# Kernel optimization log

Hardware: AMD Instinct MI355X
Metric: run time of the kernel (lower is better)

The kernel has to match this reference:

```python
import jax, jax.numpy as jnp
from jax import lax
import numpy as np

EPS = 1e-5
SCALE, K_UP = 2, 5  # CARAFE defaults


def conv(x, w, pad=0):
    return lax.conv_general_dilated(x, w, (1, 1), [(pad, pad), (pad, pad)],
                                    dimension_numbers=('NCHW', 'OIHW', 'NCHW'))


def bn(x, g, b, m, v):
    # eval-mode BatchNorm2d
    inv = g * lax.rsqrt(v + EPS)
    return x * inv[None, :, None, None] + (b - m * inv)[None, :, None, None]


def carafe(X, comp_w, comp_g, comp_bt, comp_m, comp_v, enc_w, enc_g, enc_bt, enc_m, enc_v):
    b, c, h, w = X.shape
    k2 = K_UP * K_UP
    W = jax.nn.relu(bn(conv(X, comp_w), comp_g, comp_bt, comp_m, comp_v))  # (b, c_mid, h, w)
    W = bn(conv(W, enc_w, pad=1), enc_g, enc_bt, enc_m, enc_v)             # (b, k2*SCALE^2, h, w)
    # PixelShuffle(SCALE): (b, k2*r^2, h, w) -> (b, k2, h*r, w*r)
    W = W.reshape(b, k2, SCALE, SCALE, h, w).transpose(0, 1, 4, 2, 5, 3)
    W = W.reshape(b, k2, h * SCALE, w * SCALE)
    W = jax.nn.softmax(W, axis=1)
    # nearest upsample by SCALE
    Xu = jnp.repeat(jnp.repeat(X, SCALE, axis=2), SCALE, axis=3)
    pad = (K_UP // 2) * SCALE
    Xp = jnp.pad(Xu, ((0, 0), (0, 0), (pad, pad), (pad, pad)))
    h_, w_ = h * SCALE, w * SCALE
    # Unfold(kernel=K_UP, dilation=SCALE): channel-major then kernel index, matching torch
    patches = jnp.stack([Xp[:, :, i * SCALE:i * SCALE + h_, j * SCALE:j * SCALE + w_]
                         for i in range(K_UP) for j in range(K_UP)], axis=2)  # (b,c,k2,h_,w_)
    return jnp.einsum('bkhw,bckhw->bchw', W, patches)


def setup_inputs():
    key = jax.random.key(0)
    ks = iter(jax.random.split(key, 80))
    nk = lambda: next(ks)
    P = lambda shape, s=0.05: jax.random.normal(nk(), shape, jnp.float32) * s
    d = {}
    B, C_out = 4, 64
    cins = [128, 256, 512]
    hw = [(96, 160), (48, 80), (24, 40)]
    for i, (ci, (h, w)) in enumerate(zip(cins, hw)):
        d[f'x{i}'] = jax.random.normal(nk(), (B, ci, h, w), jnp.float32)
        d[f'lat{i}_w'] = P((C_out, ci, 1, 1))
        d[f'lat{i}_b'] = P((C_out,))
        d[f'fpn{i}_w'] = P((C_out, C_out, 3, 3))
        d[f'fpn{i}_b'] = P((C_out,))
    k2s2 = (SCALE * K_UP) ** 2
    for u in range(2):
        d[f'u{u}_comp_w'] = P((C_out, C_out, 1, 1))
        d[f'u{u}_enc_w'] = P((k2s2, C_out, 3, 3))
        for nm, c in [('comp', C_out), ('enc', k2s2)]:
            d[f'u{u}_{nm}_g'] = 1.0 + P((c,))
            d[f'u{u}_{nm}_bt'] = P((c,))
            d[f'u{u}_{nm}_m'] = P((c,))
            d[f'u{u}_{nm}_v'] = jax.random.uniform(nk(), (c,), jnp.float32, 0.5, 1.5)
    return d


def reference(x0, x1, x2,
              lat0_w, lat0_b, fpn0_w, fpn0_b,
              lat1_w, lat1_b, fpn1_w, fpn1_b,
              lat2_w, lat2_b, fpn2_w, fpn2_b,
              u0_comp_w, u0_enc_w, u0_comp_g, u0_comp_bt, u0_comp_m, u0_comp_v,
              u0_enc_g, u0_enc_bt, u0_enc_m, u0_enc_v,
              u1_comp_w, u1_enc_w, u1_comp_g, u1_comp_bt, u1_comp_m, u1_comp_v,
              u1_enc_g, u1_enc_bt, u1_enc_m, u1_enc_v):
    lat = [conv(x, w) + b[None, :, None, None] for x, w, b in
           [(x0, lat0_w, lat0_b), (x1, lat1_w, lat1_b), (x2, lat2_w, lat2_b)]]
    # top-down pathway with CARAFE upsampling
    lat[1] = lat[1] + carafe(lat[2], u1_comp_w, u1_comp_g, u1_comp_bt, u1_comp_m, u1_comp_v,
                             u1_enc_w, u1_enc_g, u1_enc_bt, u1_enc_m, u1_enc_v)
    lat[0] = lat[0] + carafe(lat[1], u0_comp_w, u0_comp_g, u0_comp_bt, u0_comp_m, u0_comp_v,
                             u0_enc_w, u0_enc_g, u0_enc_bt, u0_enc_m, u0_enc_v)
    outs = tuple(conv(l, w, pad=1) + b[None, :, None, None] for l, w, b in
                 [(lat[0], fpn0_w, fpn0_b), (lat[1], fpn1_w, fpn1_b), (lat[2], fpn2_w, fpn2_b)])
    return outs
```

## Files before the change

kernel.cpp:

```cpp
#include <hip/hip_runtime.h>

#define BN_EPS 1e-5f

typedef __attribute__((ext_vector_type(8))) short bf16x8;
typedef __attribute__((ext_vector_type(4))) float f32x4;

__device__ __forceinline__ unsigned short f2bf(float f) {
    unsigned u = __float_as_uint(f);
    return (unsigned short)((u + 0x7fffu + ((u >> 16) & 1u)) >> 16);
}
__device__ __forceinline__ unsigned packbf(float lo, float hi) {
    return ((unsigned)f2bf(hi) << 16) | (unsigned)f2bf(lo);
}

__global__ __launch_bounds__(256)
void prep_weights(const float* __restrict__ w0, const float* __restrict__ w1,
                  const float* __restrict__ w2, const float* __restrict__ w3,
                  const float* __restrict__ w4, unsigned short* __restrict__ dst,
                  const float* __restrict__ v0, const float* __restrict__ v1,
                  const float* __restrict__ v2, const float* __restrict__ v3,
                  const float* __restrict__ v4, unsigned short* __restrict__ dst1)
{
    int z = blockIdx.y;
    int i = blockIdx.x * 256 + threadIdx.x;
    if (z < 5) {
        const float* src; unsigned short* d; int C_out, COP;
        if (z < 3) {
            COP = 64; C_out = 64;
            src = (z == 0) ? w0 : (z == 1 ? w1 : w2);
            d = dst + z * 36864;
            if (i >= 36864) return;
        } else {
            COP = 112; C_out = 100;
            src = (z == 3) ? w3 : w4;
            d = dst + 110592 + (z - 3) * 64512;
            if (i >= 64512) return;
        }
        int tap = i / (COP * 64);
        int rem = i - tap * (COP * 64);
        int co = rem >> 6, ci = rem & 63;
        float v = (co < C_out) ? src[((size_t)co * 64 + ci) * 9 + tap] : 0.f;
        d[i] = f2bf(v);
    } else {
        int zz = z - 5;
        const float* s; int n; int off;
        if (zz == 0)      { s = v0; n = 8192;  off = 0; }
        else if (zz == 1) { s = v1; n = 16384; off = 8192; }
        else if (zz == 2) { s = v2; n = 32768; off = 24576; }
        else if (zz == 3) { s = v3; n = 4096;  off = 57344; }
        else              { s = v4; n = 4096;  off = 61440; }
        if (i >= n) return;
        dst1[off + i] = f2bf(s[i]);
    }
}

template<int COP, int CSPLIT, int MODE>
__device__ __forceinline__
void conv3x3_body(int rem, int TX, unsigned short* xs,
                  const unsigned* __restrict__ xp,
                  const unsigned short* __restrict__ wt,
                  const float* __restrict__ p0, const float* __restrict__ p1,
                  const float* __restrict__ p2, const float* __restrict__ p3,
                  float* __restrict__ out, int H, int W, int C_out)
{
    constexpr int NP = 324;
    constexpr int CT = COP / 16;
    static_assert(CT == CSPLIT, "CPB must be 1 (R1/R2 VGPR cliff)");

    int cs = rem % CSPLIT;
    int b  = (rem / CSPLIT) & 3;
    int t  = rem / (CSPLIT * 4);
    int x0 = (t % TX) * 16, y0 = (t / TX) * 16;

    int tid  = threadIdx.x;
    int lane = tid & 63, wid = tid >> 6;
    int lrow = lane >> 4, lcol = lane & 15;
    int HWp = H * W;

    int co0 = cs * 16;
    bool colok = (x0 + lcol) < W;

    f32x4 accA[2], accB[2];
#pragma unroll
    for (int rr = 0; rr < 2; ++rr) {
        accA[rr] = (f32x4){0.f, 0.f, 0.f, 0.f};
        accB[rr] = (f32x4){0.f, 0.f, 0.f, 0.f};
    }

    unsigned int* wsl = (unsigned int*)xs;

#pragma unroll 1
    for (int kb = 0; kb < 2; ++kb) {
        if (kb) __syncthreads();
        for (int p = tid; p < NP; p += 256) {
            int py = p / 18, px = p - py * 18;
            int gy = y0 + py - 1, gx = x0 + px - 1;
            bool ok = (gy >= 0) && (gy < H) && (gx >= 0) && (gx < W);
            const unsigned* gpp = xp + ((size_t)b * 32 + kb * 16) * HWp
                                     + (size_t)gy * W + gx;
#pragma unroll 8
            for (int cp = 0; cp < 16; ++cp) {
                unsigned pk = ok ? gpp[(size_t)cp * HWp] : 0u;
                wsl[((cp >> 2) * NP + p) * 4 + (cp & 3)] = pk;
            }
        }
        __syncthreads();

        bf16x8 a[9];
        const unsigned short* wl = wt + ((size_t)co0 + lcol) * 64 + kb * 32 + lrow * 8;
#pragma unroll
        for (int t9 = 0; t9 < 9; ++t9)
            a[t9] = *(const bf16x8*)(wl + (size_t)t9 * COP * 64);

#pragma unroll
        for (int rr = 0; rr < 2; ++rr) {
            int r0 = wid + rr * 8;
#pragma unroll
            for (int t9 = 0; t9 < 9; ++t9) {
                int dy = t9 / 3, dx = t9 - dy * 3;
                int g0 = lrow * NP + (r0 + dy) * 18 + lcol + dx;
                bf16x8 b0 = *(const bf16x8*)(xs + (size_t)g0 * 8);
                accA[rr] = __builtin_amdgcn_mfma_f32_16x16x32_bf16(a[t9], b0, accA[rr], 0, 0, 0);
                bf16x8 b1 = *(const bf16x8*)(xs + ((size_t)g0 + 4 * 18) * 8);
                accB[rr] = __builtin_amdgcn_mfma_f32_16x16x32_bf16(a[t9], b1, accB[rr], 0, 0, 0);
            }
        }
    }

    float sc[4], sh[4];
#pragma unroll
    for (int rg = 0; rg < 4; ++rg) {
        int co = co0 + lrow * 4 + rg;
        int cc = (co < C_out) ? co : 0;
        if (MODE == 0) { sc[rg] = 1.f; sh[rg] = p0[cc]; }
        else {
            float inv = p0[cc] * rsqrtf(p3[cc] + BN_EPS);
            sc[rg] = inv; sh[rg] = p1[cc] - p2[cc] * inv;
        }
    }
#pragma unroll
    for (int rr = 0; rr < 2; ++rr) {
        int r0 = wid + rr * 8;
        int yA = y0 + r0, yB = y0 + r0 + 4;
#pragma unroll
        for (int rg = 0; rg < 4; ++rg) {
            int co = co0 + lrow * 4 + rg;
            if (colok && co < C_out) {
                float* oc = out + (((size_t)b * C_out + co) * H) * W + x0 + lcol;
                if (yA < H) oc[(size_t)yA * W] = accA[rr][rg] * sc[rg] + sh[rg];
                if (yB < H) oc[(size_t)yB * W] = accB[rr][rg] * sc[rg] + sh[rg];
            }
        }
    }
}

__global__ __launch_bounds__(256, 6)
void enc_fpn(int encBlocks,
             const unsigned* __restrict__ cxp, const unsigned short* __restrict__ wt_e,
             const float* __restrict__ g, const float* __restrict__ bt,
             const float* __restrict__ m, const float* __restrict__ v,
             float* __restrict__ enc_out, int He, int We, int TXe,
             const unsigned* __restrict__ xp, const unsigned short* __restrict__ wt_f,
             const float* __restrict__ bias, float* __restrict__ fout,
             int Hf, int Wf, int TXf)
{
    __shared__ unsigned short xs[4 * 324 * 8];
    int f = blockIdx.x;
    if (f < encBlocks)
        conv3x3_body<112, 7, 1>(f, TXe, xs, cxp, wt_e,
                                g, bt, m, v, enc_out, He, We, 100);
    else
        conv3x3_body<64, 4, 0>(f - encBlocks, TXf, xs, xp, wt_f,
                               bias, nullptr, nullptr, nullptr, fout, Hf, Wf, 64);
}

__global__ __launch_bounds__(256, 6)
void fpn_multi(const unsigned* __restrict__ l0p, const unsigned short* __restrict__ wt0,
               const float* __restrict__ b0, float* __restrict__ o0)
{
    __shared__ unsigned short xs[4 * 324 * 8];
    conv3x3_body<64, 4, 0>(blockIdx.x, 10, xs, l0p, wt0,
                           b0, nullptr, nullptr, nullptr, o0, 96, 160, 64);
}

template<int C_IN, int KSPLIT, int NPX, int MODE, bool MIRROR>
__device__ __forceinline__
void conv1x1_body(int f, unsigned short* xs,
                  const float* __restrict__ x, const unsigned short* __restrict__ wb,
                  const float* __restrict__ p0, const float* __restrict__ p1,
                  const float* __restrict__ p2, const float* __restrict__ p3,
                  float* __restrict__ out, unsigned* __restrict__ outp, int HW)
{
    constexpr int NT = NPX / 16;
    constexpr int KLEN = C_IN / KSPLIT;
    constexpr int QUADS = NPX / 4;
    int nb = HW / NPX;
    int px0 = (f % nb) * NPX;
    int ks  = (f / nb) % KSPLIT;
    int b   = f / (nb * KSPLIT);

    int tid = threadIdx.x;
    int lane = tid & 63, wid = tid >> 6;
    int lrow = lane >> 4, lcol = lane & 15;
    const float* xb = x + (size_t)b * C_IN * HW + px0;

    f32x4 acc[NT];
#pragma unroll
    for (int nt = 0; nt < NT; ++nt) acc[nt] = (f32x4){0.f, 0.f, 0.f, 0.f};

    for (int cc = 0; cc < KLEN; cc += 32) {
        if (cc) __syncthreads();
        int cb = ks * KLEN + cc;
        for (int j = tid; j < 16 * QUADS; j += 256) {
            int q  = j & (QUADS - 1);
            int cp = j / QUADS;
            int px = q * 4;
            const float* s0 = xb + (size_t)(cb + 2 * cp) * HW + px;
            float4 v0 = *(const float4*)s0;
            float4 v1 = *(const float4*)(s0 + HW);
            unsigned* wv = (unsigned*)xs + ((size_t)(cp >> 2) * NPX + px) * 4 + (cp & 3);
            wv[0]  = packbf(v0.x, v1.x);
            wv[4]  = packbf(v0.y, v1.y);
            wv[8]  = packbf(v0.z, v1.z);
            wv[12] = packbf(v0.w, v1.w);
        }
        __syncthreads();

        bf16x8 a = *(const bf16x8*)(wb + (size_t)(wid * 16 + lcol) * C_IN + cb + lrow * 8);
#pragma unroll
        for (int nt = 0; nt < NT; ++nt) {
            bf16x8 bf = *(const bf16x8*)(xs + ((size_t)lrow * NPX + nt * 16 + lcol) * 8);
            acc[nt] = __builtin_amdgcn_mfma_f32_16x16x32_bf16(a, bf, acc[nt], 0, 0, 0);
        }
    }

    if (KSPLIT == 1) {
        if (MIRROR) {
#pragma unroll
            for (int rg = 0; rg < 4; rg += 2) {
                int co = wid * 16 + lrow * 4 + rg;
                float inv0 = p0[co] * rsqrtf(p3[co] + BN_EPS);
                float sh0  = p1[co] - p2[co] * inv0;
                float inv1 = p0[co + 1] * rsqrtf(p3[co + 1] + BN_EPS);
                float sh1  = p1[co + 1] - p2[co + 1] * inv1;
                unsigned* pp = outp + ((size_t)(b * 32 + (co >> 1))) * HW + px0;
#pragma unroll
                for (int nt = 0; nt < NT; ++nt) {
                    float r0 = fmaxf(acc[nt][rg] * inv0 + sh0, 0.f);
                    float r1 = fmaxf(acc[nt][rg + 1] * inv1 + sh1, 0.f);
                    pp[nt * 16 + lcol] = packbf(r0, r1);
                }
            }
        } else {
#pragma unroll
            for (int rg = 0; rg < 4; ++rg) {
                int co = wid * 16 + lrow * 4 + rg;
                float scale, shift;
                if (MODE == 0) { scale = 1.f; shift = p0[co]; }
                else {
                    float inv = p0[co] * rsqrtf(p3[co] + BN_EPS);
                    scale = inv; shift = p1[co] - p2[co] * inv;
                }
                float* op = out + ((size_t)(b * 64 + co)) * HW + px0;
#pragma unroll
                for (int nt = 0; nt < NT; ++nt) {
                    float r = acc[nt][rg] * scale + shift;
                    if (MODE == 1) r = fmaxf(r, 0.f);
                    op[nt * 16 + lcol] = r;
                }
            }
        }
    } else {
#pragma unroll
        for (int rg = 0; rg < 4; ++rg) {
            int co = wid * 16 + lrow * 4 + rg;
            float* op = out + (((size_t)(ks * 4 + b)) * 64 + co) * HW + px0;
#pragma unroll
            for (int nt = 0; nt < NT; ++nt)
                op[nt * 16 + lcol] = acc[nt][rg];
        }
    }
}

template<int C_IN, int KSPLIT, int NPX, int MODE, bool MIRROR>
__global__ __launch_bounds__(256, 4)
void conv1x1_mfma(const float* __restrict__ x, const unsigned short* __restrict__ wb,
                  const float* __restrict__ p0, const float* __restrict__ p1,
                  const float* __restrict__ p2, const float* __restrict__ p3,
                  float* __restrict__ out, unsigned* __restrict__ outp, int HW)
{
    __shared__ __align__(16) unsigned short xs[4 * NPX * 8];
    int nb = HW / NPX;
    int f = blockIdx.x + nb * (blockIdx.y + KSPLIT * blockIdx.z);
    conv1x1_body<C_IN, KSPLIT, NPX, MODE, MIRROR>(f, xs, x, wb, p0, p1, p2, p3, out, outp, HW);
}

__global__ __launch_bounds__(256, 4)
void lat_multi(const float* __restrict__ x0, const unsigned short* __restrict__ w0,
               const float* __restrict__ b0, float* __restrict__ lat0,
               const float* __restrict__ x1, const unsigned short* __restrict__ w1,
               float* __restrict__ part1,
               const float* __restrict__ x2, const unsigned short* __restrict__ w2,
               float* __restrict__ part2)
{
    __shared__ __align__(16) unsigned short xs[4 * 128 * 8];
    int f = blockIdx.x;
    if (f < 480)
        conv1x1_body<128, 1, 128, 0, false>(f, xs, x0, w0, b0, nullptr, nullptr, nullptr, lat0, nullptr, 15360);
    else if (f < 720)
        conv1x1_body<256, 2, 128, 0, false>(f - 480, xs, x1, w1, nullptr, nullptr, nullptr, nullptr, part1, nullptr, 3840);
    else
        conv1x1_body<512, 4, 64, 0, false>(f - 720, xs, x2, w2, nullptr, nullptr, nullptr, nullptr, part2, nullptr, 960);
}

template<int KSPLIT>
__device__ __forceinline__
void reduce_body(int f, const float* __restrict__ part, const float* __restrict__ bias,
                 float* __restrict__ out, int HW, int N4)
{
    int i = f * 256 + threadIdx.x;
    if (i >= N4) return;
    size_t base = (size_t)i * 4;
    int co = (int)((base / (size_t)HW) & 63);
    size_t stride = (size_t)HW << 8;
    float4 s = *(const float4*)(part + base);
#pragma unroll
    for (int ks = 1; ks < KSPLIT; ++ks) {
        float4 t = *(const float4*)(part + (size_t)ks * stride + base);
        s.x += t.x; s.y += t.y; s.z += t.z; s.w += t.w;
    }
    float bv = bias[co];
    s.x += bv; s.y += bv; s.z += bv; s.w += bv;
    *(float4*)(out + base) = s;
}

__device__ __forceinline__
void reduce_pack4(int f, const float* __restrict__ part, const float* __restrict__ bias,
                  float* __restrict__ out, unsigned* __restrict__ outp, int HW, int N)
{
    int i = f * 256 + threadIdx.x;
    if (i >= N) return;
    int q = HW >> 2;
    int pxq  = i % q;
    int rest = i / q;
    int cp = rest & 31, b = rest >> 5;
    size_t off = (size_t)pxq * 4;
    size_t c0 = ((size_t)(b * 64 + 2 * cp)) * HW + off;
    size_t stride = (size_t)HW << 8;
    float4 s0 = *(const float4*)(part + c0);
    float4 s1 = *(const float4*)(part + c0 + HW);
#pragma unroll
    for (int ks = 1; ks < 4; ++ks) {
        float4 t0 = *(const float4*)(part + (size_t)ks * stride + c0);
        float4 t1 = *(const float4*)(part + (size_t)ks * stride + c0 + HW);
        s0.x += t0.x; s0.y += t0.y; s0.z += t0.z; s0.w += t0.w;
        s1.x += t1.x; s1.y += t1.y; s1.z += t1.z; s1.w += t1.w;
    }
    float bv0 = bias[2 * cp], bv1 = bias[2 * cp + 1];
    s0.x += bv0; s0.y += bv0; s0.z += bv0; s0.w += bv0;
    s1.x += bv1; s1.y += bv1; s1.z += bv1; s1.w += bv1;
    *(float4*)(out + c0) = s0;
    *(float4*)(out + c0 + HW) = s1;
    uint4 pk;
    pk.x = packbf(s0.x, s1.x);
    pk.y = packbf(s0.y, s1.y);
    pk.z = packbf(s0.z, s1.z);
    pk.w = packbf(s0.w, s1.w);
    *(uint4*)(outp + ((size_t)(b * 32 + cp)) * HW + off) = pk;
}

__global__ __launch_bounds__(256)
void reduce_multi(const float* __restrict__ part1, const float* __restrict__ b1,
                  float* __restrict__ lat1,
                  const float* __restrict__ part2, const float* __restrict__ b2,
                  float* __restrict__ lat2, unsigned* __restrict__ lat2p)
{
    int f = blockIdx.x;
    if (f < 960) reduce_body<2>(f, part1, b1, lat1, 3840, 245760);
    else         reduce_pack4(f - 960, part2, b2, lat2, lat2p, 960, 30720);
}

template<int CGS, bool WF32>
__global__ __launch_bounds__(256, 4)
void carafe_kernel(const float* __restrict__ src, const float* __restrict__ logits,
                   float* __restrict__ dst, unsigned* __restrict__ dstp, int h, int w)
{
    constexpr int SW = 12, NPX = 144;
    constexpr int CH = 64 / CGS;
    constexpr int CS = CH + 4;
    __shared__ float ls[NPX * CS];

    int tid = threadIdx.x;
    int x0 = blockIdx.x * 16, y0 = blockIdx.y * 16;
    int b  = blockIdx.z / CGS;
    int cs = blockIdx.z % CGS;
    int H = 2 * h, W = 2 * w;
    int xs0 = (x0 >> 1) - 2, ys0 = (y0 >> 1) - 2;
    size_t hw = (size_t)h * w;
    const float* sb = src + ((size_t)(b * 64 + cs * CH)) * hw;

    for (int i = tid; i < NPX * CH; i += 256) {
        int c = i / NPX, p = i - c * NPX;
        int yy = p / SW, xx = p - yy * SW;
        int sy = ys0 + yy, sx = xs0 + xx;
        float v = 0.f;
        if (sy >= 0 && sy < h && sx >= 0 && sx < w)
            v = sb[(size_t)c * hw + (size_t)sy * w + sx];
        ls[p * CS + c] = v;
    }
    __syncthreads();

    int lx = tid & 15, ty = tid >> 4;
    int x = x0 + lx, y = y0 + ty;
    int xw = x >> 1, yh = y >> 1;
    int par = (y & 1) * 2 + (x & 1);

    const float* lp = logits + ((size_t)(b * 100 + par) * h + yh) * w + xw;
    float l[25];
    float mx = -1e30f;
#pragma unroll
    for (int k = 0; k < 25; ++k) {
        l[k] = lp[(size_t)(4 * k) * hw];
        mx = fmaxf(mx, l[k]);
    }
    float s = 0.f;
#pragma unroll
    for (int k = 0; k < 25; ++k) {
        l[k] = __expf(l[k] - mx);
        s += l[k];
    }
    float invs = 1.f / s;
#pragma unroll
    for (int k = 0; k < 25; ++k) l[k] *= invs;

    int pb = (yh - ys0 - 2) * SW + (xw - xs0 - 2);

#pragma unroll 1
    for (int cg = 0; cg < CH / 16; ++cg) {
        float acc[16];
#pragma unroll
        for (int c = 0; c < 16; ++c) acc[c] = 0.f;
#pragma unroll
        for (int k = 0; k < 25; ++k) {
            int ti = k / 5, tj = k - ti * 5;
            const float* q = &ls[(pb + ti * SW + tj) * CS + cg * 16];
            float wk = l[k];
#pragma unroll
            for (int c = 0; c < 16; ++c)
                acc[c] = fmaf(wk, q[c], acc[c]);
        }
        int cbase = cs * CH + cg * 16;
        float* dp = dst + (((size_t)(b * 64 + cbase)) * H + y) * W + x;
        unsigned* pp = dstp + (((size_t)(b * 32 + (cbase >> 1))) * H + y) * W + x;
#pragma unroll
        for (int c = 0; c < 16; c += 2) {
            float n0 = dp[(size_t)c * H * W] + acc[c];
            float n1 = dp[(size_t)(c + 1) * H * W] + acc[c + 1];
            if (WF32) {
                dp[(size_t)c * H * W] = n0;
                dp[(size_t)(c + 1) * H * W] = n1;
            }
            pp[(size_t)(c >> 1) * H * W] = packbf(n0, n1);
        }
    }
}

extern "C" void kernel_launch(void* const* d_in, const int* in_sizes, int n_in,
                              void* d_out, int out_size, void* d_ws, size_t ws_size,
                              hipStream_t stream)
{
    const float* x0      = (const float*)d_in[0];
    const float* lat0_w  = (const float*)d_in[1];
    const float* lat0_b  = (const float*)d_in[2];
    const float* fpn0_w  = (const float*)d_in[3];
    const float* fpn0_b  = (const float*)d_in[4];
    const float* x1      = (const float*)d_in[5];
    const float* lat1_w  = (const float*)d_in[6];
    const float* lat1_b  = (const float*)d_in[7];
    const float* fpn1_w  = (const float*)d_in[8];
    const float* fpn1_b  = (const float*)d_in[9];
    const float* x2      = (const float*)d_in[10];
    const float* lat2_w  = (const float*)d_in[11];
    const float* lat2_b  = (const float*)d_in[12];
    const float* fpn2_w  = (const float*)d_in[13];
    const float* fpn2_b  = (const float*)d_in[14];
    const float* u0_comp_w = (const float*)d_in[15];
    const float* u0_enc_w  = (const float*)d_in[16];
    const float* u0_comp_g  = (const float*)d_in[17];
    const float* u0_comp_bt = (const float*)d_in[18];
    const float* u0_comp_m  = (const float*)d_in[19];
    const float* u0_comp_v  = (const float*)d_in[20];
    const float* u0_enc_g   = (const float*)d_in[21];
    const float* u0_enc_bt  = (const float*)d_in[22];
    const float* u0_enc_m   = (const float*)d_in[23];
    const float* u0_enc_v   = (const float*)d_in[24];
    const float* u1_comp_w = (const float*)d_in[25];
    const float* u1_enc_w  = (const float*)d_in[26];
    const float* u1_comp_g  = (const float*)d_in[27];
    const float* u1_comp_bt = (const float*)d_in[28];
    const float* u1_comp_m  = (const float*)d_in[29];
    const float* u1_comp_v  = (const float*)d_in[30];
    const float* u1_enc_g   = (const float*)d_in[31];
    const float* u1_enc_bt  = (const float*)d_in[32];
    const float* u1_enc_m   = (const float*)d_in[33];
    const float* u1_enc_v   = (const float*)d_in[34];

    float* out = (float*)d_out;
    const size_t OUT0 = 4ull * 64 * 96 * 160;
    const size_t OUT1 = 4ull * 64 * 48 * 80;
    const size_t OUT2 = 4ull * 64 * 24 * 40;
    float* out0 = out;
    float* out1 = out + OUT0;
    float* out2 = out + OUT0 + OUT1;

    float* lat0 = (float*)d_ws;
    float* lat1 = lat0 + OUT0;
    float* lat2 = lat1 + OUT1;
    unsigned short* wtb = (unsigned short*)(lat2 + OUT2);
    unsigned short* wt_fpn0 = wtb;
    unsigned short* wt_fpn1 = wtb + 36864;
    unsigned short* wt_fpn2 = wtb + 73728;
    unsigned short* wt_enc0 = wtb + 110592;
    unsigned short* wt_enc1 = wtb + 175104;
    unsigned short* wb = wtb + 239616;
    unsigned short* wb_lat0  = wb;
    unsigned short* wb_lat1  = wb + 8192;
    unsigned short* wb_lat2  = wb + 24576;
    unsigned short* wb_comp0 = wb + 57344;
    unsigned short* wb_comp1 = wb + 61440;
    unsigned* lat0p = (unsigned*)(wb + 65536);
    unsigned* lat1p = lat0p + 1966080;
    unsigned* lat2p = lat1p + 491520;
    unsigned* compp = lat2p + 122880;
    float* part1 = out0;
    float* part2 = out0 + 2 * OUT1;
    float* enc   = out0 + OUT1;

    dim3 blk(256);

    prep_weights<<<dim3(252, 10), blk, 0, stream>>>(
        fpn0_w, fpn1_w, fpn2_w, u0_enc_w, u1_enc_w, wtb,
        lat0_w, lat1_w, lat2_w, u0_comp_w, u1_comp_w, wb);

    lat_multi<<<dim3(960), blk, 0, stream>>>(
        x0, wb_lat0, lat0_b, lat0, x1, wb_lat1, part1, x2, wb_lat2, part2);

    reduce_multi<<<dim3(1080), blk, 0, stream>>>(
        part1, lat1_b, lat1, part2, lat2_b, lat2, lat2p);

    conv1x1_mfma<64, 1, 32, 1, true><<<dim3(30, 1, 4), blk, 0, stream>>>(
        lat2, wb_comp1, u1_comp_g, u1_comp_bt, u1_comp_m, u1_comp_v, nullptr, compp, 24 * 40);
    enc_fpn<<<dim3(264), blk, 0, stream>>>(168,
        compp, wt_enc1, u1_enc_g, u1_enc_bt, u1_enc_m, u1_enc_v, enc, 24, 40, 3,
        lat2p, wt_fpn2, fpn2_b, out2, 24, 40, 3);
    carafe_kernel<2, true><<<dim3(5, 3, 8), blk, 0, stream>>>(lat2, enc, lat1, lat1p, 24, 40);

    conv1x1_mfma<64, 1, 32, 1, true><<<dim3(120, 1, 4), blk, 0, stream>>>(
        lat1, wb_comp0, u0_comp_g, u0_comp_bt, u0_comp_m, u0_comp_v, nullptr, compp, 48 * 80);
    enc_fpn<<<dim3(660), blk, 0, stream>>>(420,
        compp, wt_enc0, u0_enc_g, u0_enc_bt, u0_enc_m, u0_enc_v, enc, 48, 80, 5,
        lat1p, wt_fpn1, fpn1_b, out1, 48, 80, 5);
    carafe_kernel<2, false><<<dim3(10, 6, 8), blk, 0, stream>>>(lat1, enc, lat0, lat0p, 48, 80);

    fpn_multi<<<dim3(960), blk, 0, stream>>>(lat0p, wt_fpn0, fpn0_b, out0);
}
```

Before: 287.2 us.

## Drop split-K lateral convs and reduce kernel; feed CARAFE and comp convs packed bf16

The lateral 1x1 convs for levels 1 and 2 now run without split-K, so the partial-sum buffers and the separate reduce kernel go away. Level 2 writes only packed bf16. The comp convs and the CARAFE kernels now read the packed bf16 copies instead of fp32, and CARAFE no longer writes an fp32 copy of lat1. This removes one launch and several fp32 round trips through memory. In exchange, fewer blocks run for levels 1 and 2, and source features are rounded to bf16 before CARAFE and comp.

```diff
diff --git a/kernel.cpp b/kernel.cpp
--- a/kernel.cpp
+++ b/kernel.cpp
@@ -183,50 +183,54 @@
                            b0, nullptr, nullptr, nullptr, o0, 96, 160, 64);
 }
 
-template<int C_IN, int KSPLIT, int NPX, int MODE, bool MIRROR>
+template<int C_IN, int NPX, int MODE, bool INPK, bool OUTMIR>
 __device__ __forceinline__
 void conv1x1_body(int f, unsigned short* xs,
-                  const float* __restrict__ x, const unsigned short* __restrict__ wb,
+                  const float* __restrict__ x, const unsigned* __restrict__ xp,
+                  const unsigned short* __restrict__ wb,
                   const float* __restrict__ p0, const float* __restrict__ p1,
                   const float* __restrict__ p2, const float* __restrict__ p3,
                   float* __restrict__ out, unsigned* __restrict__ outp, int HW)
 {
     constexpr int NT = NPX / 16;
-    constexpr int KLEN = C_IN / KSPLIT;
     constexpr int QUADS = NPX / 4;
     int nb = HW / NPX;
     int px0 = (f % nb) * NPX;
-    int ks  = (f / nb) % KSPLIT;
-    int b   = f / (nb * KSPLIT);
+    int b   = f / nb;
 
     int tid = threadIdx.x;
     int lane = tid & 63, wid = tid >> 6;
     int lrow = lane >> 4, lcol = lane & 15;
-    const float* xb = x + (size_t)b * C_IN * HW + px0;
+    const float*    xb  = INPK ? nullptr : x + (size_t)b * C_IN * HW + px0;
+    const unsigned* xpb = INPK ? xp + (size_t)b * (C_IN / 2) * HW + px0 : nullptr;
 
     f32x4 acc[NT];
 #pragma unroll
     for (int nt = 0; nt < NT; ++nt) acc[nt] = (f32x4){0.f, 0.f, 0.f, 0.f};
 
-    for (int cc = 0; cc < KLEN; cc += 32) {
+    for (int cc = 0; cc < C_IN; cc += 32) {
         if (cc) __syncthreads();
-        int cb = ks * KLEN + cc;
         for (int j = tid; j < 16 * QUADS; j += 256) {
             int q  = j & (QUADS - 1);
             int cp = j / QUADS;
             int px = q * 4;
-            const float* s0 = xb + (size_t)(cb + 2 * cp) * HW + px;
-            float4 v0 = *(const float4*)s0;
-            float4 v1 = *(const float4*)(s0 + HW);
             unsigned* wv = (unsigned*)xs + ((size_t)(cp >> 2) * NPX + px) * 4 + (cp & 3);
-            wv[0]  = packbf(v0.x, v1.x);
-            wv[4]  = packbf(v0.y, v1.y);
-            wv[8]  = packbf(v0.z, v1.z);
-            wv[12] = packbf(v0.w, v1.w);
+            if (INPK) {
+                uint4 v = *(const uint4*)(xpb + (size_t)(cc / 2 + cp) * HW + px);
+                wv[0] = v.x; wv[4] = v.y; wv[8] = v.z; wv[12] = v.w;
+            } else {
+                const float* s0 = xb + (size_t)(cc + 2 * cp) * HW + px;
+                float4 v0 = *(const float4*)s0;
+                float4 v1 = *(const float4*)(s0 + HW);
+                wv[0]  = packbf(v0.x, v1.x);
+                wv[4]  = packbf(v0.y, v1.y);
+                wv[8]  = packbf(v0.z, v1.z);
+                wv[12] = packbf(v0.w, v1.w);
+            }
         }
         __syncthreads();
 
-        bf16x8 a = *(const bf16x8*)(wb + (size_t)(wid * 16 + lcol) * C_IN + cb + lrow * 8);
+        bf16x8 a = *(const bf16x8*)(wb + (size_t)(wid * 16 + lcol) * C_IN + cc + lrow * 8);
 #pragma unroll
         for (int nt = 0; nt < NT; ++nt) {
             bf16x8 bf = *(const bf16x8*)(xs + ((size_t)lrow * NPX + nt * 16 + lcol) * 8);
@@ -234,159 +238,92 @@
         }
     }
 
-    if (KSPLIT == 1) {
-        if (MIRROR) {
-#pragma unroll
-            for (int rg = 0; rg < 4; rg += 2) {
-                int co = wid * 16 + lrow * 4 + rg;
-                float inv0 = p0[co] * rsqrtf(p3[co] + BN_EPS);
-                float sh0  = p1[co] - p2[co] * inv0;
-                float inv1 = p0[co + 1] * rsqrtf(p3[co + 1] + BN_EPS);
-                float sh1  = p1[co + 1] - p2[co + 1] * inv1;
-                unsigned* pp = outp + ((size_t)(b * 32 + (co >> 1))) * HW + px0;
-#pragma unroll
-                for (int nt = 0; nt < NT; ++nt) {
-                    float r0 = fmaxf(acc[nt][rg] * inv0 + sh0, 0.f);
-                    float r1 = fmaxf(acc[nt][rg + 1] * inv1 + sh1, 0.f);
-                    pp[nt * 16 + lcol] = packbf(r0, r1);
-                }
-            }
-        } else {
-#pragma unroll
-            for (int rg = 0; rg < 4; ++rg) {
-                int co = wid * 16 + lrow * 4 + rg;
-                float scale, shift;
-                if (MODE == 0) { scale = 1.f; shift = p0[co]; }
-                else {
-                    float inv = p0[co] * rsqrtf(p3[co] + BN_EPS);
-                    scale = inv; shift = p1[co] - p2[co] * inv;
-                }
-                float* op = out + ((size_t)(b * 64 + co)) * HW + px0;
-#pragma unroll
-                for (int nt = 0; nt < NT; ++nt) {
-                    float r = acc[nt][rg] * scale + shift;
-                    if (MODE == 1) r = fmaxf(r, 0.f);
-                    op[nt * 16 + lcol] = r;
-                }
+    if (OUTMIR) {
+#pragma unroll
+        for (int rg = 0; rg < 4; rg += 2) {
+            int co = wid * 16 + lrow * 4 + rg;
+            float s0, h0, s1, h1;
+            if (MODE == 0) { s0 = 1.f; h0 = p0[co]; s1 = 1.f; h1 = p0[co + 1]; }
+            else {
+                s0 = p0[co] * rsqrtf(p3[co] + BN_EPS);
+                h0 = p1[co] - p2[co] * s0;
+                s1 = p0[co + 1] * rsqrtf(p3[co + 1] + BN_EPS);
+                h1 = p1[co + 1] - p2[co + 1] * s1;
+            }
+            unsigned* pp = outp + ((size_t)(b * 32 + (co >> 1))) * HW + px0;
+#pragma unroll
+            for (int nt = 0; nt < NT; ++nt) {
+                float r0 = acc[nt][rg] * s0 + h0;
+                float r1 = acc[nt][rg + 1] * s1 + h1;
+                if (MODE == 1) { r0 = fmaxf(r0, 0.f); r1 = fmaxf(r1, 0.f); }
+                pp[nt * 16 + lcol] = packbf(r0, r1);
             }
         }
     } else {
 #pragma unroll
         for (int rg = 0; rg < 4; ++rg) {
             int co = wid * 16 + lrow * 4 + rg;
-            float* op = out + (((size_t)(ks * 4 + b)) * 64 + co) * HW + px0;
-#pragma unroll
-            for (int nt = 0; nt < NT; ++nt)
-                op[nt * 16 + lcol] = acc[nt][rg];
-        }
-    }
-}
-
-template<int C_IN, int KSPLIT, int NPX, int MODE, bool MIRROR>
+            float scale, shift;
+            if (MODE == 0) { scale = 1.f; shift = p0[co]; }
+            else {
+                float inv = p0[co] * rsqrtf(p3[co] + BN_EPS);
+                scale = inv; shift = p1[co] - p2[co] * inv;
+            }
+            float* op = out + ((size_t)(b * 64 + co)) * HW + px0;
+#pragma unroll
+            for (int nt = 0; nt < NT; ++nt) {
+                float r = acc[nt][rg] * scale + shift;
+                if (MODE == 1) r = fmaxf(r, 0.f);
+                op[nt * 16 + lcol] = r;
+            }
+        }
+    }
+}
+
+template<int C_IN, int NPX, int MODE, bool INPK, bool OUTMIR>
 __global__ __launch_bounds__(256, 4)
-void conv1x1_mfma(const float* __restrict__ x, const unsigned short* __restrict__ wb,
+void conv1x1_mfma(const float* __restrict__ x, const unsigned* __restrict__ xp,
+                  const unsigned short* __restrict__ wb,
                   const float* __restrict__ p0, const float* __restrict__ p1,
                   const float* __restrict__ p2, const float* __restrict__ p3,
                   float* __restrict__ out, unsigned* __restrict__ outp, int HW)
 {
     __shared__ __align__(16) unsigned short xs[4 * NPX * 8];
     int nb = HW / NPX;
-    int f = blockIdx.x + nb * (blockIdx.y + KSPLIT * blockIdx.z);
-    conv1x1_body<C_IN, KSPLIT, NPX, MODE, MIRROR>(f, xs, x, wb, p0, p1, p2, p3, out, outp, HW);
+    int f = blockIdx.x + nb * blockIdx.z;
+    conv1x1_body<C_IN, NPX, MODE, INPK, OUTMIR>(f, xs, x, xp, wb, p0, p1, p2, p3, out, outp, HW);
 }
 
 __global__ __launch_bounds__(256, 4)
 void lat_multi(const float* __restrict__ x0, const unsigned short* __restrict__ w0,
                const float* __restrict__ b0, float* __restrict__ lat0,
                const float* __restrict__ x1, const unsigned short* __restrict__ w1,
-               float* __restrict__ part1,
+               const float* __restrict__ b1, float* __restrict__ lat1,
                const float* __restrict__ x2, const unsigned short* __restrict__ w2,
-               float* __restrict__ part2)
+               const float* __restrict__ b2, unsigned* __restrict__ lat2p)
 {
     __shared__ __align__(16) unsigned short xs[4 * 128 * 8];
     int f = blockIdx.x;
     if (f < 480)
-        conv1x1_body<128, 1, 128, 0, false>(f, xs, x0, w0, b0, nullptr, nullptr, nullptr, lat0, nullptr, 15360);
-    else if (f < 720)
-        conv1x1_body<256, 2, 128, 0, false>(f - 480, xs, x1, w1, nullptr, nullptr, nullptr, nullptr, part1, nullptr, 3840);
+        conv1x1_body<128, 128, 0, false, false>(f, xs, x0, nullptr, w0,
+            b0, nullptr, nullptr, nullptr, lat0, nullptr, 15360);
+    else if (f < 600)
+        conv1x1_body<256, 128, 0, false, false>(f - 480, xs, x1, nullptr, w1,
+            b1, nullptr, nullptr, nullptr, lat1, nullptr, 3840);
     else
-        conv1x1_body<512, 4, 64, 0, false>(f - 720, xs, x2, w2, nullptr, nullptr, nullptr, nullptr, part2, nullptr, 960);
-}
-
-template<int KSPLIT>
-__device__ __forceinline__
-void reduce_body(int f, const float* __restrict__ part, const float* __restrict__ bias,
-                 float* __restrict__ out, int HW, int N4)
-{
-    int i = f * 256 + threadIdx.x;
-    if (i >= N4) return;
-    size_t base = (size_t)i * 4;
-    int co = (int)((base / (size_t)HW) & 63);
-    size_t stride = (size_t)HW << 8;
-    float4 s = *(const float4*)(part + base);
-#pragma unroll
-    for (int ks = 1; ks < KSPLIT; ++ks) {
-        float4 t = *(const float4*)(part + (size_t)ks * stride + base);
-        s.x += t.x; s.y += t.y; s.z += t.z; s.w += t.w;
-    }
-    float bv = bias[co];
-    s.x += bv; s.y += bv; s.z += bv; s.w += bv;
-    *(float4*)(out + base) = s;
-}
-
-__device__ __forceinline__
-void reduce_pack4(int f, const float* __restrict__ part, const float* __restrict__ bias,
-                  float* __restrict__ out, unsigned* __restrict__ outp, int HW, int N)
-{
-    int i = f * 256 + threadIdx.x;
-    if (i >= N) return;
-    int q = HW >> 2;
-    int pxq  = i % q;
-    int rest = i / q;
-    int cp = rest & 31, b = rest >> 5;
-    size_t off = (size_t)pxq * 4;
-    size_t c0 = ((size_t)(b * 64 + 2 * cp)) * HW + off;
-    size_t stride = (size_t)HW << 8;
-    float4 s0 = *(const float4*)(part + c0);
-    float4 s1 = *(const float4*)(part + c0 + HW);
-#pragma unroll
-    for (int ks = 1; ks < 4; ++ks) {
-        float4 t0 = *(const float4*)(part + (size_t)ks * stride + c0);
-        float4 t1 = *(const float4*)(part + (size_t)ks * stride + c0 + HW);
-        s0.x += t0.x; s0.y += t0.y; s0.z += t0.z; s0.w += t0.w;
-        s1.x += t1.x; s1.y += t1.y; s1.z += t1.z; s1.w += t1.w;
-    }
-    float bv0 = bias[2 * cp], bv1 = bias[2 * cp + 1];
-    s0.x += bv0; s0.y += bv0; s0.z += bv0; s0.w += bv0;
-    s1.x += bv1; s1.y += bv1; s1.z += bv1; s1.w += bv1;
-    *(float4*)(out + c0) = s0;
-    *(float4*)(out + c0 + HW) = s1;
-    uint4 pk;
-    pk.x = packbf(s0.x, s1.x);
-    pk.y = packbf(s0.y, s1.y);
-    pk.z = packbf(s0.z, s1.z);
-    pk.w = packbf(s0.w, s1.w);
-    *(uint4*)(outp + ((size_t)(b * 32 + cp)) * HW + off) = pk;
-}
-
-__global__ __launch_bounds__(256)
-void reduce_multi(const float* __restrict__ part1, const float* __restrict__ b1,
-                  float* __restrict__ lat1,
-                  const float* __restrict__ part2, const float* __restrict__ b2,
-                  float* __restrict__ lat2, unsigned* __restrict__ lat2p)
-{
-    int f = blockIdx.x;
-    if (f < 960) reduce_body<2>(f, part1, b1, lat1, 3840, 245760);
-    else         reduce_pack4(f - 960, part2, b2, lat2, lat2p, 960, 30720);
-}
-
-template<int CGS, bool WF32>
+        conv1x1_body<512, 64, 0, false, true>(f - 600, xs, x2, nullptr, w2,
+            b2, nullptr, nullptr, nullptr, nullptr, lat2p, 960);
+}
+
+template<int CGS>
 __global__ __launch_bounds__(256, 4)
-void carafe_kernel(const float* __restrict__ src, const float* __restrict__ logits,
-                   float* __restrict__ dst, unsigned* __restrict__ dstp, int h, int w)
+void carafe_kernel(const unsigned* __restrict__ srcp, const float* __restrict__ logits,
+                   const float* __restrict__ base, unsigned* __restrict__ dstp,
+                   int h, int w)
 {
     constexpr int SW = 12, NPX = 144;
     constexpr int CH = 64 / CGS;
+    constexpr int CP = CH / 2;
     constexpr int CS = CH + 4;
     __shared__ float ls[NPX * CS];
 
@@ -397,16 +334,17 @@
     int H = 2 * h, W = 2 * w;
     int xs0 = (x0 >> 1) - 2, ys0 = (y0 >> 1) - 2;
     size_t hw = (size_t)h * w;
-    const float* sb = src + ((size_t)(b * 64 + cs * CH)) * hw;
-
-    for (int i = tid; i < NPX * CH; i += 256) {
-        int c = i / NPX, p = i - c * NPX;
+    const unsigned* sb = srcp + ((size_t)(b * 32 + cs * CP)) * hw;
+
+    for (int i = tid; i < NPX * CP; i += 256) {
+        int cpl = i / NPX, p = i - cpl * NPX;
         int yy = p / SW, xx = p - yy * SW;
         int sy = ys0 + yy, sx = xs0 + xx;
-        float v = 0.f;
+        unsigned u = 0;
         if (sy >= 0 && sy < h && sx >= 0 && sx < w)
-            v = sb[(size_t)c * hw + (size_t)sy * w + sx];
-        ls[p * CS + c] = v;
+            u = sb[(size_t)cpl * hw + (size_t)sy * w + sx];
+        ls[p * CS + 2 * cpl]     = __uint_as_float(u << 16);
+        ls[p * CS + 2 * cpl + 1] = __uint_as_float(u & 0xffff0000u);
     }
     __syncthreads();
 
@@ -450,16 +388,12 @@
                 acc[c] = fmaf(wk, q[c], acc[c]);
         }
         int cbase = cs * CH + cg * 16;
-        float* dp = dst + (((size_t)(b * 64 + cbase)) * H + y) * W + x;
+        const float* dp = base + (((size_t)(b * 64 + cbase)) * H + y) * W + x;
         unsigned* pp = dstp + (((size_t)(b * 32 + (cbase >> 1))) * H + y) * W + x;
 #pragma unroll
         for (int c = 0; c < 16; c += 2) {
             float n0 = dp[(size_t)c * H * W] + acc[c];
             float n1 = dp[(size_t)(c + 1) * H * W] + acc[c + 1];
-            if (WF32) {
-                dp[(size_t)c * H * W] = n0;
-                dp[(size_t)(c + 1) * H * W] = n1;
-            }
             pp[(size_t)(c >> 1) * H * W] = packbf(n0, n1);
         }
     }
@@ -532,8 +466,6 @@
     unsigned* lat1p = lat0p + 1966080;
     unsigned* lat2p = lat1p + 491520;
     unsigned* compp = lat2p + 122880;
-    float* part1 = out0;
-    float* part2 = out0 + 2 * OUT1;
     float* enc   = out0 + OUT1;
 
     dim3 blk(256);
@@ -542,25 +474,26 @@
         fpn0_w, fpn1_w, fpn2_w, u0_enc_w, u1_enc_w, wtb,
         lat0_w, lat1_w, lat2_w, u0_comp_w, u1_comp_w, wb);
 
-    lat_multi<<<dim3(960), blk, 0, stream>>>(
-        x0, wb_lat0, lat0_b, lat0, x1, wb_lat1, part1, x2, wb_lat2, part2);
-
-    reduce_multi<<<dim3(1080), blk, 0, stream>>>(
-        part1, lat1_b, lat1, part2, lat2_b, lat2, lat2p);
-
-    conv1x1_mfma<64, 1, 32, 1, true><<<dim3(30, 1, 4), blk, 0, stream>>>(
-        lat2, wb_comp1, u1_comp_g, u1_comp_bt, u1_comp_m, u1_comp_v, nullptr, compp, 24 * 40);
+    lat_multi<<<dim3(660), blk, 0, stream>>>(
+        x0, wb_lat0, lat0_b, lat0,
+        x1, wb_lat1, lat1_b, lat1,
+        x2, wb_lat2, lat2_b, lat2p);
+
+    conv1x1_mfma<64, 32, 1, true, true><<<dim3(30, 1, 4), blk, 0, stream>>>(
+        nullptr, lat2p, wb_comp1, u1_comp_g, u1_comp_bt, u1_comp_m, u1_comp_v,
+        nullptr, compp, 24 * 40);
     enc_fpn<<<dim3(264), blk, 0, stream>>>(168,
         compp, wt_enc1, u1_enc_g, u1_enc_bt, u1_enc_m, u1_enc_v, enc, 24, 40, 3,
         lat2p, wt_fpn2, fpn2_b, out2, 24, 40, 3);
-    carafe_kernel<2, true><<<dim3(5, 3, 8), blk, 0, stream>>>(lat2, enc, lat1, lat1p, 24, 40);
-
-    conv1x1_mfma<64, 1, 32, 1, true><<<dim3(120, 1, 4), blk, 0, stream>>>(
-        lat1, wb_comp0, u0_comp_g, u0_comp_bt, u0_comp_m, u0_comp_v, nullptr, compp, 48 * 80);
+    carafe_kernel<2><<<dim3(5, 3, 8), blk, 0, stream>>>(lat2p, enc, lat1, lat1p, 24, 40);
+
+    conv1x1_mfma<64, 32, 1, true, true><<<dim3(120, 1, 4), blk, 0, stream>>>(
+        nullptr, lat1p, wb_comp0, u0_comp_g, u0_comp_bt, u0_comp_m, u0_comp_v,
+        nullptr, compp, 48 * 80);
     enc_fpn<<<dim3(660), blk, 0, stream>>>(420,
         compp, wt_enc0, u0_enc_g, u0_enc_bt, u0_enc_m, u0_enc_v, enc, 48, 80, 5,
         lat1p, wt_fpn1, fpn1_b, out1, 48, 80, 5);
-    carafe_kernel<2, false><<<dim3(10, 6, 8), blk, 0, stream>>>(lat1, enc, lat0, lat0p, 48, 80);
+    carafe_kernel<2><<<dim3(10, 6, 8), blk, 0, stream>>>(lat1p, enc, lat0, lat0p, 48, 80);
 
     fpn_multi<<<dim3(960), blk, 0, stream>>>(lat0p, wt_fpn0, fpn0_b, out0);
 }
```

New measurement: 276.2 us. 3.8% less time.
